# Kernel tuning notes

Measured on AMD Instinct MI355X. Metric: run time of the kernel, lower is better.

Reference implementation:

```python
import jax, jax.numpy as jnp
import numpy as np

IN_FEATURES = 4096
OUT_FEATURES = 4096
RANK = 8
ALPHA = 16
SCALING = ALPHA / RANK  # 2.0


def setup_inputs() -> dict:
    key = jax.random.key(0)
    kx, ka, kb = jax.random.split(key, 3)
    x = jax.random.normal(kx, (4, 4096, IN_FEATURES), dtype=jnp.float32)
    # A ~ randn as in the torch init; B is zeros in torch but we use small randn
    # so the output/grads are non-trivial for correctness testing.
    A = jax.random.normal(ka, (RANK, OUT_FEATURES), dtype=jnp.float32)
    B = jax.random.normal(kb, (IN_FEATURES, RANK), dtype=jnp.float32) * 0.02
    return {"x": x, "A": A, "B": B}


def reference(x, A, B):
    # Faithful math: scaling * (dropout(x) @ (B @ A)); dropout p=0.0 -> identity.
    # Original materializes the full [in, out] matrix B @ A before the GEMM.
    BA = jnp.matmul(B, A)  # [in_features, out_features]
    return SCALING * jnp.matmul(x, BA)  # [batch, seq, out_features]
```

## Files before the change

kernel.cpp:

```cpp
#include <hip/hip_runtime.h>


#define NT      256
#define ROWS    16
#define KDIM    4096
#define NDIM    4096
#define M_TOTAL 16384

typedef __attribute__((ext_vector_type(4))) float float4v;

__global__ __launch_bounds__(NT, 2) void lora_fused(
    const float* __restrict__ x,
    const float* __restrict__ A,
    const float* __restrict__ B,
    float* __restrict__ out)
{
    __shared__ float part[ROWS][4][8];
    __shared__ float tl[ROWS][8];

    const int t = threadIdx.x;
    const int lane = t & 63;
    const int wave = t >> 6;
    const long m_base = (long)blockIdx.x * ROWS;

    float frag[16][8];

    {
        const float4v* Bv = (const float4v*)B;
#pragma unroll
        for (int q = 0; q < 4; ++q)
#pragma unroll
            for (int i = 0; i < 4; ++i) {
                const int k = q * 1024 + 4 * t + i;
                float4v b0 = Bv[2 * k];
                float4v b1 = Bv[2 * k + 1];
                const int j = 4 * q + i;
#pragma unroll
                for (int r = 0; r < 4; ++r) {
                    frag[j][r]     = b0[r];
                    frag[j][4 + r] = b1[r];
                }
            }
    }

    float4v c0[4], c1[4];
    {
        const float4v* x0 = (const float4v*)(x + m_base * KDIM);
        const float4v* x1 = (const float4v*)(x + (m_base + 1) * KDIM);
#pragma unroll
        for (int q = 0; q < 4; ++q) {
            c0[q] = x0[q * 256 + t];
            c1[q] = x1[q * 256 + t];
        }
    }

    auto p1_body = [&](float4v (&cb)[4], int rr) {
        float acc[8];
#pragma unroll
        for (int r = 0; r < 8; ++r) acc[r] = 0.0f;
#pragma unroll
        for (int q = 0; q < 4; ++q)
#pragma unroll
            for (int i = 0; i < 4; ++i) {
                const float xv = cb[q][i];
                const int j = 4 * q + i;
#pragma unroll
                for (int r = 0; r < 8; ++r)
                    acc[r] = fmaf(xv, frag[j][r], acc[r]);
            }

        const int nr = rr + 2;
        if (nr < ROWS) {
            const float4v* xn = (const float4v*)(x + (m_base + nr) * KDIM);
#pragma unroll
            for (int q = 0; q < 4; ++q) cb[q] = xn[q * 256 + t];
        }

        float s[8];
#pragma unroll
        for (int r = 0; r < 8; ++r) s[r] = __shfl_xor(acc[r], 32, 64);
        const bool b5 = (lane & 32) != 0;
        float v[4];
#pragma unroll
        for (int j = 0; j < 4; ++j)
            v[j] = b5 ? (acc[4 + j] + s[4 + j]) : (acc[j] + s[j]);
        float sb[4];
#pragma unroll
        for (int j = 0; j < 4; ++j) sb[j] = __shfl_xor(v[j], 16, 64);
        const bool b4 = (lane & 16) != 0;
        float w0 = b4 ? (v[2] + sb[2]) : (v[0] + sb[0]);
        float w1 = b4 ? (v[3] + sb[3]) : (v[1] + sb[1]);
        float sc0 = __shfl_xor(w0, 8, 64);
        float sc1 = __shfl_xor(w1, 8, 64);
        const bool b3 = (lane & 8) != 0;
        float u = b3 ? (w1 + sc1) : (w0 + sc0);
        u += __shfl_xor(u, 4, 64);
        u += __shfl_xor(u, 2, 64);
        u += __shfl_xor(u, 1, 64);
        if ((lane & 7) == 0) {
            const int r = (((lane >> 5) & 1) << 2) | (((lane >> 4) & 1) << 1) |
                          ((lane >> 3) & 1);
            part[rr][wave][r] = u;
        }
    };

#pragma unroll 1
    for (int rp = 0; rp < ROWS; rp += 2) {
        p1_body(c0, rp);
        p1_body(c1, rp + 1);
    }

    __syncthreads();
    if (t < ROWS * 8) {
        const int rr = t >> 3, r = t & 7;
        tl[rr][r] = 2.0f * (part[rr][0][r] + part[rr][1][r] +
                            part[rr][2][r] + part[rr][3][r]);
    }

    {
        const float4v* Av = (const float4v*)A;
#pragma unroll
        for (int r = 0; r < 8; ++r)
#pragma unroll
            for (int q = 0; q < 4; ++q) {
                float4v a = Av[r * 1024 + q * 256 + t];
#pragma unroll
                for (int i = 0; i < 4; ++i)
                    frag[4 * q + i][r] = a[i];
            }
    }
    __syncthreads();

#pragma unroll 2
    for (int rr = 0; rr < ROWS; ++rr) {
        float tv[8];
#pragma unroll
        for (int r = 0; r < 8; ++r) tv[r] = tl[rr][r];

        float4v* orow = (float4v*)(out + (m_base + rr) * NDIM);
#pragma unroll
        for (int q = 0; q < 4; ++q) {
            float4v o;
#pragma unroll
            for (int i = 0; i < 4; ++i) {
                float s2 = 0.0f;
#pragma unroll
                for (int r = 0; r < 8; ++r)
                    s2 = fmaf(tv[r], frag[4 * q + i][r], s2);
                o[i] = s2;
            }
            orow[q * 256 + t] = o;
        }
    }
}

extern "C" void kernel_launch(void* const* d_in, const int* in_sizes, int n_in,
                              void* d_out, int out_size, void* d_ws, size_t ws_size,
                              hipStream_t stream) {
    const float* x = (const float*)d_in[0];
    const float* A = (const float*)d_in[1];
    const float* B = (const float*)d_in[2];
    float* out = (float*)d_out;

    (void)in_sizes; (void)n_in; (void)out_size; (void)d_ws; (void)ws_size;

    dim3 grid(M_TOTAL / ROWS);
    lora_fused<<<grid, NT, 0, stream>>>(x, A, B, out);
}
```

Measured before the change: 444.9 us.

## Split fused LoRA kernel into x@B and t@A kernels with K-split partials

```diff
diff --git a/kernel.cpp b/kernel.cpp
--- a/kernel.cpp
+++ b/kernel.cpp
@@ -1,80 +1,62 @@
 #include <hip/hip_runtime.h>
 
 
-#define NT      256
-#define ROWS    16
 #define KDIM    4096
 #define NDIM    4096
 #define M_TOTAL 16384
+#define K1_ROWS 32
+#define K2_ROWS 32
+#define NPART   16
 
 typedef __attribute__((ext_vector_type(4))) float float4v;
 
-__global__ __launch_bounds__(NT, 2) void lora_fused(
+__global__ __launch_bounds__(256, 4) void lora_xb(
     const float* __restrict__ x,
-    const float* __restrict__ A,
     const float* __restrict__ B,
-    float* __restrict__ out)
+    float* __restrict__ tpart)
 {
-    __shared__ float part[ROWS][4][8];
-    __shared__ float tl[ROWS][8];
-
-    const int t = threadIdx.x;
+    const int t    = threadIdx.x;
     const int lane = t & 63;
     const int wave = t >> 6;
-    const long m_base = (long)blockIdx.x * ROWS;
+    const int bid  = blockIdx.x;
+    const int kb   = bid & 3;
+    const int rg   = bid >> 2;
+    const long m0  = (long)rg * K1_ROWS;
+    const int kbase = kb * 1024 + 4 * t;
+    const int p    = kb * 4 + wave;
 
-    float frag[16][8];
-
+    float fb[4][8];
     {
         const float4v* Bv = (const float4v*)B;
 #pragma unroll
-        for (int q = 0; q < 4; ++q)
+        for (int i = 0; i < 4; ++i) {
+            float4v b0 = Bv[2 * (kbase + i)];
+            float4v b1 = Bv[2 * (kbase + i) + 1];
 #pragma unroll
-            for (int i = 0; i < 4; ++i) {
-                const int k = q * 1024 + 4 * t + i;
-                float4v b0 = Bv[2 * k];
-                float4v b1 = Bv[2 * k + 1];
-                const int j = 4 * q + i;
-#pragma unroll
-                for (int r = 0; r < 4; ++r) {
-                    frag[j][r]     = b0[r];
-                    frag[j][4 + r] = b1[r];
-                }
-            }
-    }
-
-    float4v c0[4], c1[4];
-    {
-        const float4v* x0 = (const float4v*)(x + m_base * KDIM);
-        const float4v* x1 = (const float4v*)(x + (m_base + 1) * KDIM);
-#pragma unroll
-        for (int q = 0; q < 4; ++q) {
-            c0[q] = x0[q * 256 + t];
-            c1[q] = x1[q * 256 + t];
+            for (int r = 0; r < 4; ++r) { fb[i][r] = b0[r]; fb[i][4 + r] = b1[r]; }
         }
     }
 
-    auto p1_body = [&](float4v (&cb)[4], int rr) {
+    float4v c0, c1, c2, c3;
+    c0 = *(const float4v*)(x + (m0 + 0) * KDIM + kbase);
+    c1 = *(const float4v*)(x + (m0 + 1) * KDIM + kbase);
+    c2 = *(const float4v*)(x + (m0 + 2) * KDIM + kbase);
+    c3 = *(const float4v*)(x + (m0 + 3) * KDIM + kbase);
+
+    auto body = [&](float4v& cb, int rr) {
         float acc[8];
 #pragma unroll
         for (int r = 0; r < 8; ++r) acc[r] = 0.0f;
 #pragma unroll
-        for (int q = 0; q < 4; ++q)
+        for (int i = 0; i < 4; ++i) {
+            const float xv = cb[i];
 #pragma unroll
-            for (int i = 0; i < 4; ++i) {
-                const float xv = cb[q][i];
-                const int j = 4 * q + i;
-#pragma unroll
-                for (int r = 0; r < 8; ++r)
-                    acc[r] = fmaf(xv, frag[j][r], acc[r]);
-            }
-
-        const int nr = rr + 2;
-        if (nr < ROWS) {
-            const float4v* xn = (const float4v*)(x + (m_base + nr) * KDIM);
-#pragma unroll
-            for (int q = 0; q < 4; ++q) cb[q] = xn[q * 256 + t];
+            for (int r = 0; r < 8; ++r)
+                acc[r] = fmaf(xv, fb[i][r], acc[r]);
         }
+        const int nr = rr + 4;
+        if (nr < K1_ROWS)
+            cb = *(const float4v*)(x + (m0 + nr) * KDIM + kbase);
 
         float s[8];
 #pragma unroll
@@ -100,57 +82,63 @@
         if ((lane & 7) == 0) {
             const int r = (((lane >> 5) & 1) << 2) | (((lane >> 4) & 1) << 1) |
                           ((lane >> 3) & 1);
-            part[rr][wave][r] = u;
+            tpart[((m0 + rr) * NPART + p) * 8 + r] = u;
         }
     };
 
 #pragma unroll 1
-    for (int rp = 0; rp < ROWS; rp += 2) {
-        p1_body(c0, rp);
-        p1_body(c1, rp + 1);
+    for (int rp = 0; rp < K1_ROWS; rp += 4) {
+        body(c0, rp);
+        body(c1, rp + 1);
+        body(c2, rp + 2);
+        body(c3, rp + 3);
     }
+}
 
-    __syncthreads();
-    if (t < ROWS * 8) {
-        const int rr = t >> 3, r = t & 7;
-        tl[rr][r] = 2.0f * (part[rr][0][r] + part[rr][1][r] +
-                            part[rr][2][r] + part[rr][3][r]);
-    }
+__global__ __launch_bounds__(256, 4) void lora_ta(
+    const float* __restrict__ tpart,
+    const float* __restrict__ A,
+    float* __restrict__ out)
+{
+    __shared__ float tl[K2_ROWS][8];
+
+    const int t   = threadIdx.x;
+    const int bid = blockIdx.x;
+    const int nb  = bid & 3;
+    const int rg  = bid >> 2;
+    const long m0 = (long)rg * K2_ROWS;
+    const int n0  = nb * 1024 + 4 * t;
+
+    float4v fa[8];
+#pragma unroll
+    for (int r = 0; r < 8; ++r)
+        fa[r] = *(const float4v*)(A + r * NDIM + n0);
 
     {
-        const float4v* Av = (const float4v*)A;
+        const int mm = t >> 3, r = t & 7;
+        const float* tp = tpart + ((m0 + mm) * NPART) * 8 + r;
+        float s = 0.0f;
 #pragma unroll
-        for (int r = 0; r < 8; ++r)
-#pragma unroll
-            for (int q = 0; q < 4; ++q) {
-                float4v a = Av[r * 1024 + q * 256 + t];
-#pragma unroll
-                for (int i = 0; i < 4; ++i)
-                    frag[4 * q + i][r] = a[i];
-            }
+        for (int pp = 0; pp < NPART; ++pp) s += tp[pp * 8];
+        tl[mm][r] = 2.0f * s;
     }
     __syncthreads();
 
 #pragma unroll 2
-    for (int rr = 0; rr < ROWS; ++rr) {
+    for (int mm = 0; mm < K2_ROWS; ++mm) {
         float tv[8];
 #pragma unroll
-        for (int r = 0; r < 8; ++r) tv[r] = tl[rr][r];
-
-        float4v* orow = (float4v*)(out + (m_base + rr) * NDIM);
+        for (int r = 0; r < 8; ++r) tv[r] = tl[mm][r];
+        float4v o;
 #pragma unroll
-        for (int q = 0; q < 4; ++q) {
-            float4v o;
+        for (int i = 0; i < 4; ++i) {
+            float s = 0.0f;
 #pragma unroll
-            for (int i = 0; i < 4; ++i) {
-                float s2 = 0.0f;
-#pragma unroll
-                for (int r = 0; r < 8; ++r)
-                    s2 = fmaf(tv[r], frag[4 * q + i][r], s2);
-                o[i] = s2;
-            }
-            orow[q * 256 + t] = o;
+            for (int r = 0; r < 8; ++r)
+                s = fmaf(tv[r], fa[r][i], s);
+            o[i] = s;
         }
+        *(float4v*)(out + (m0 + mm) * NDIM + n0) = o;
     }
 }
 
@@ -161,9 +149,12 @@
     const float* A = (const float*)d_in[1];
     const float* B = (const float*)d_in[2];
     float* out = (float*)d_out;
+    float* tpart = (float*)d_ws;
 
-    (void)in_sizes; (void)n_in; (void)out_size; (void)d_ws; (void)ws_size;
+    (void)in_sizes; (void)n_in; (void)out_size; (void)ws_size;
 
-    dim3 grid(M_TOTAL / ROWS);
-    lora_fused<<<grid, NT, 0, stream>>>(x, A, B, out);
+    dim3 g1(4 * (M_TOTAL / K1_ROWS));
+    dim3 g2(4 * (M_TOTAL / K2_ROWS));
+    lora_xb<<<g1, 256, 0, stream>>>(x, B, tpart);
+    lora_ta<<<g2, 256, 0, stream>>>(tpart, A, out);
 }
```

Measured after the change: 462.3 us. +3.9%, slower.
